# Kernel optimization log

Hardware: AMD Instinct MI355X
Metric: run time of the kernel (lower is better)

The kernel has to match this reference:

```python
import jax, jax.numpy as jnp
import numpy as np

B, N, L, D = 4, 32, 64, 512      # batch, num_nodes, his_len, input_dim
H, O = 1024, 512                  # expert hidden, output_dim
E, S, TOP_K = 16, 3, 2            # independent experts, shared experts, top-k


def setup_inputs() -> dict:
    key = jax.random.key(0)
    ks = jax.random.split(key, 12)
    sc = 0.02
    return {
        "feature_vectors": jax.random.normal(ks[0], (B, N, L, D), jnp.float32),
        "object_types": jax.random.uniform(ks[1], (B, N, L, S, 1), jnp.float32),
        "gating_w": jax.random.normal(ks[2], (D, E), jnp.float32) * sc,
        "gating_b": jnp.zeros((E,), jnp.float32),
        "sh_w1": jax.random.normal(ks[3], (S, D, H), jnp.float32) * sc,
        "sh_b1": jnp.zeros((S, H), jnp.float32),
        "sh_w2": jax.random.normal(ks[4], (S, H, O), jnp.float32) * sc,
        "sh_b2": jnp.zeros((S, O), jnp.float32),
        "ind_w1": jax.random.normal(ks[5], (E, D, H), jnp.float32) * sc,
        "ind_b1": jnp.zeros((E, H), jnp.float32),
        "ind_w2": jax.random.normal(ks[6], (E, H, O), jnp.float32) * sc,
        "ind_b2": jnp.zeros((E, O), jnp.float32),
    }


def reference(feature_vectors, object_types, gating_w, gating_b,
              sh_w1, sh_b1, sh_w2, sh_b2,
              ind_w1, ind_b1, ind_w2, ind_b2):
    b, n, l, d = feature_vectors.shape
    x = feature_vectors.reshape(-1, d)                       # [T, D]
    T = x.shape[0]

    # gating: softmax -> top-k -> renormalize selected weights
    gating = jax.nn.softmax(x @ gating_w + gating_b, axis=-1)  # [T, E]
    vals, idx = jax.lax.top_k(gating, TOP_K)                   # [T, K]
    w = vals / vals.sum(axis=-1, keepdims=True)                # [T, K]

    # shared experts: per-type FFN, weighted by object_types
    obj = object_types.reshape(-1, S, 1)                       # [T, S, 1]
    sh_h = jax.nn.relu(jnp.einsum('td,sdh->tsh', x, sh_w1) + sh_b1)
    sh_o = jnp.einsum('tsh,sho->tso', sh_h, sh_w2) + sh_b2     # [T, S, O]
    shared_out = (sh_o * obj).sum(axis=1)                      # [T, O]

    # independent experts: dense all-expert compute, combine via top-k weights
    # (equivalent to the bincount/mask dispatch loop: unselected experts get 0)
    ind_h = jax.nn.relu(jnp.einsum('td,edh->teh', x, ind_w1) + ind_b1)
    ind_o = jnp.einsum('teh,eho->teo', ind_h, ind_w2) + ind_b2  # [T, E, O]
    comb = jnp.zeros((T, gating_w.shape[1]), x.dtype)
    comb = comb.at[jnp.arange(T)[:, None], idx].add(w)          # [T, E] sparse weights
    ind_out = jnp.einsum('te,teo->to', comb, ind_o)             # [T, O]

    out = 0.5 * shared_out + 0.5 * ind_out
    return out.reshape(b, n, l, -1)
```

## Files before the change

kernel.cpp:

```cpp
#include <hip/hip_runtime.h>
#include <hip/hip_bf16.h>
#include <stdint.h>

#define T_TOK 8192
#define DIM   512
#define HID   1024
#define ODIM  512
#define NEXP  16
#define NSH   3

#define BM 128
#define BN 128
#define BK 64
#define MAXTILES 144
#define CAPSLOTS (MAXTILES * BM)

typedef __attribute__((ext_vector_type(8))) short s16x8;
typedef __attribute__((ext_vector_type(4))) float f32x4;

__device__ __forceinline__ uint16_t f2bf(float f) {
  union { float f; uint32_t u; } x; x.f = f;
  uint32_t r = x.u + 0x7FFFu + ((x.u >> 16) & 1u);
  return (uint16_t)(r >> 16);
}
__device__ __forceinline__ float bf2f(uint16_t u) {
  union { uint32_t u; float f; } x; x.u = ((uint32_t)u) << 16;
  return x.f;
}

__device__ __forceinline__ void async_copy16(const uint16_t* g, uint16_t* l) {
  __builtin_amdgcn_global_load_lds(
      (const __attribute__((address_space(1))) void*)g,
      (__attribute__((address_space(3))) void*)l, 16, 0, 0);
}

__global__ __launch_bounds__(256) void k_cvt_all(
    const float* __restrict__ shw1, const float* __restrict__ shw2,
    const float* __restrict__ iw1, const float* __restrict__ iw2,
    uint16_t* __restrict__ shw1T, uint16_t* __restrict__ shw2T,
    uint16_t* __restrict__ iw1T, uint16_t* __restrict__ iw2T) {
  __shared__ float tl[64][68];
  int id = blockIdx.x;
  const float* src; uint16_t* dst; int K, N, ldk; size_t dz;
  if (id < 384)       { src = shw1; dst = shw1T; K = 512;  N = 1024; dz = (size_t)HID * DIM;  ldk = 512; }
  else if (id < 768)  { src = shw2; dst = shw2T; K = 1024; N = 512;  dz = HID;                ldk = 3072; id -= 384; }
  else if (id < 2816) { src = iw1;  dst = iw1T;  K = 512;  N = 1024; dz = (size_t)HID * DIM;  ldk = 512;  id -= 768; }
  else                { src = iw2;  dst = iw2T;  K = 1024; N = 512;  dz = (size_t)ODIM * HID; ldk = 1024; id -= 2816; }
  int z = id >> 7, tile = id & 127;
  int ntn = N >> 6;
  int n0 = (tile & (ntn - 1)) * 64, k0 = (tile / ntn) * 64;
  src += (size_t)z * K * N;
  dst += (size_t)z * dz;
  int tid = threadIdx.x;
  int lr = tid >> 4, lc = (tid & 15) * 4;
#pragma unroll
  for (int p = 0; p < 4; ++p) {
    int row = lr + p * 16;
    float4 v = *(const float4*)&src[(size_t)(k0 + row) * N + n0 + lc];
    tl[row][lc + 0] = v.x; tl[row][lc + 1] = v.y;
    tl[row][lc + 2] = v.z; tl[row][lc + 3] = v.w;
  }
  __syncthreads();
  int nr = tid >> 3, kc = (tid & 7) * 8;
#pragma unroll
  for (int p = 0; p < 2; ++p) {
    int n = nr + p * 32;
    s16x8 o;
#pragma unroll
    for (int j = 0; j < 8; ++j) o[j] = (short)f2bf(tl[kc + j][n]);
    *(s16x8*)&dst[(size_t)(n0 + n) * ldk + k0 + kc] = o;
  }
}

#define GTPB 16
__global__ __launch_bounds__(256) void k_gating(const float* __restrict__ x,
                                                const float* __restrict__ gw,
                                                const float* __restrict__ gb,
                                                uint16_t* __restrict__ xb,
                                                int* __restrict__ tok_top,
                                                float* __restrict__ wgt_top,
                                                int* __restrict__ cnt) {
  __shared__ float xs[GTPB][516];
  __shared__ float gws[NEXP][516];
  __shared__ int hist[NEXP];
  int tid = threadIdx.x;
  int tb = blockIdx.x * GTPB;
  if (tid < NEXP) hist[tid] = 0;
#pragma unroll
  for (int it = 0; it < 8; ++it) {
    int idx = (it * 256 + tid) * 4;
    float4 v = *(const float4*)&gw[idx];
    int d = idx >> 4, e0 = idx & 15;
    gws[e0 + 0][d] = v.x; gws[e0 + 1][d] = v.y;
    gws[e0 + 2][d] = v.z; gws[e0 + 3][d] = v.w;
  }
#pragma unroll
  for (int it = 0; it < 8; ++it) {
    int idx = it * 1024 + tid * 4;
    float4 v = *(const float4*)&x[(size_t)tb * DIM + idx];
    *(float4*)&xs[idx >> 9][idx & 511] = v;
  }
  __syncthreads();
#pragma unroll
  for (int it = 0; it < 4; ++it) {
    int idx = it * 2048 + tid * 8;
    int row = idx >> 9, col = idx & 511;
    float4 v0 = *(const float4*)&xs[row][col];
    float4 v1 = *(const float4*)&xs[row][col + 4];
    ushort4 o0, o1;
    o0.x = f2bf(v0.x); o0.y = f2bf(v0.y); o0.z = f2bf(v0.z); o0.w = f2bf(v0.w);
    o1.x = f2bf(v1.x); o1.y = f2bf(v1.y); o1.z = f2bf(v1.z); o1.w = f2bf(v1.w);
    *(ushort4*)&xb[(size_t)(tb + row) * DIM + col] = o0;
    *(ushort4*)&xb[(size_t)(tb + row) * DIM + col + 4] = o1;
  }
  int tok = tid >> 4, e = tid & 15;
  float acc = 0.f;
#pragma unroll 8
  for (int k = 0; k < DIM / 4; ++k) {
    float4 xv = *(const float4*)&xs[tok][k * 4];
    float4 gv = *(const float4*)&gws[e][k * 4];
    acc += xv.x * gv.x + xv.y * gv.y + xv.z * gv.z + xv.w * gv.w;
  }
  acc += gb[e];
  int lbase = (tid & 63) & 48;
  float best1 = -3.4e38f; int i1 = 0;
#pragma unroll
  for (int ee = 0; ee < NEXP; ++ee) {
    float v = __shfl(acc, lbase + ee, 64);
    if (v > best1) { best1 = v; i1 = ee; }
  }
  float best2 = -3.4e38f; int i2 = 0;
#pragma unroll
  for (int ee = 0; ee < NEXP; ++ee) {
    float v = __shfl(acc, lbase + ee, 64);
    if (ee != i1 && v > best2) { best2 = v; i2 = ee; }
  }
  if (e == 0) {
    int t = tb + tok;
    float w0 = 1.f / (1.f + expf(best2 - best1));
    tok_top[t * 2] = i1; tok_top[t * 2 + 1] = i2;
    wgt_top[t * 2] = w0; wgt_top[t * 2 + 1] = 1.f - w0;
    atomicAdd(&hist[i1], 1);
    atomicAdd(&hist[i2], 1);
  }
  __syncthreads();
  if (tid < NEXP && hist[tid]) atomicAdd(&cnt[tid], hist[tid]);
}

__global__ __launch_bounds__(256) void k_sched(const int* __restrict__ cnt,
                                               int* __restrict__ eoff,
                                               int* __restrict__ tdesc,
                                               int* __restrict__ ntl,
                                               int* __restrict__ rowtok,
                                               int* __restrict__ fill) {
  if (threadIdx.x == 0) {
    int o = 0, nt = 0;
    for (int e = 0; e < NEXP; ++e) {
      eoff[e] = o;
      int c = cnt[e];
      int t = (c + BM - 1) >> 7;
      for (int i = 0; i < t; ++i) { tdesc[nt * 2] = e; tdesc[nt * 2 + 1] = o + i * BM; ++nt; }
      o += t << 7;
      fill[e] = 0;
    }
    eoff[NEXP] = o;
    *ntl = nt;
  }
  for (int i = threadIdx.x; i < CAPSLOTS; i += 256) rowtok[i] = -1;
}

__global__ __launch_bounds__(256) void k_fill(const int* __restrict__ tok_top,
                                              const int* __restrict__ eoff,
                                              int* __restrict__ fill,
                                              int* __restrict__ rowtok,
                                              int* __restrict__ tok2slot) {
  int t = blockIdx.x * 256 + threadIdx.x;
  if (t >= T_TOK) return;
#pragma unroll
  for (int k = 0; k < 2; ++k) {
    int e = tok_top[t * 2 + k];
    int p = atomicAdd(&fill[e], 1);
    int slot = eoff[e] + p;
    rowtok[slot] = t;
    tok2slot[t * 2 + k] = slot;
  }
}

__device__ __forceinline__ void gemm_core(
    const uint16_t* a0, const uint16_t* a1, const uint16_t* a2, const uint16_t* a3,
    const uint16_t* b0, const uint16_t* b1, const uint16_t* b2, const uint16_t* b3,
    int nsteps, uint16_t* As, uint16_t* Bs, int wlds,
    int tl, int th, int wr, int wc, f32x4 (&acc)[4][4]) {
  const int sw = (tl & 7) << 3;
  for (int ks = 0; ks < nsteps; ++ks) {
    async_copy16(a0, As + wlds);           async_copy16(a1, As + wlds + 8 * BK);
    async_copy16(a2, As + wlds + 16 * BK); async_copy16(a3, As + wlds + 24 * BK);
    async_copy16(b0, Bs + wlds);           async_copy16(b1, Bs + wlds + 8 * BK);
    async_copy16(b2, Bs + wlds + 16 * BK); async_copy16(b3, Bs + wlds + 24 * BK);
    __syncthreads();
#pragma unroll
    for (int kk = 0; kk < 2; ++kk) {
      s16x8 af[4], bf[4];
#pragma unroll
      for (int i = 0; i < 4; ++i) {
        int eo = (kk * 32 + th * 8) ^ sw;
        af[i] = *(const s16x8*)&As[(wr * 64 + i * 16 + tl) * BK + eo];
        bf[i] = *(const s16x8*)&Bs[(wc * 64 + i * 16 + tl) * BK + eo];
      }
#pragma unroll
      for (int i = 0; i < 4; ++i)
#pragma unroll
        for (int j = 0; j < 4; ++j)
          acc[i][j] = __builtin_amdgcn_mfma_f32_16x16x32_bf16(af[i], bf[j], acc[i][j], 0, 0, 0);
    }
    __syncthreads();
    a0 += BK; a1 += BK; a2 += BK; a3 += BK;
    b0 += BK; b1 += BK; b2 += BK; b3 += BK;
  }
}

__global__ __launch_bounds__(256) void k_mega1(
    const uint16_t* __restrict__ xb, const uint16_t* __restrict__ shw1T,
    const float* __restrict__ shb1, const float* __restrict__ obj,
    uint16_t* __restrict__ hbuf,
    const int* __restrict__ tdesc, const int* __restrict__ ntl,
    const int* __restrict__ rowtok, const uint16_t* __restrict__ iw1T,
    const float* __restrict__ ib1, uint16_t* __restrict__ hind) {
  __shared__ uint16_t As[BM * BK], Bs[BN * BK];
  int id = blockIdx.x;
  int tid = threadIdx.x, lane = tid & 63, wid = tid >> 6;
  int wr = wid >> 1, wc = wid & 1, tl = lane & 15, th = lane >> 4;
  int lr = wid * 32 + (lane >> 3), koff = ((lane & 7) ^ (lane >> 3)) * 8;
  int wlds = wid * 32 * BK;
  f32x4 acc[4][4] = {};
  if (id < 1536) {
    int xcd = id & 7, g = id >> 3;
    int m0 = (xcd * 8 + g / 24) * BM;
    int n0 = (g % 24) * BN;
    const uint16_t* a0 = xb + (size_t)(m0 + lr) * DIM + koff;
    const uint16_t* b0 = shw1T + (size_t)(n0 + lr) * DIM + koff;
    gemm_core(a0, a0 + 8 * DIM, a0 + 16 * DIM, a0 + 24 * DIM,
              b0, b0 + 8 * DIM, b0 + 16 * DIM, b0 + 24 * DIM,
              DIM / BK, As, Bs, wlds, tl, th, wr, wc, acc);
#pragma unroll
    for (int i = 0; i < 4; ++i)
#pragma unroll
      for (int j = 0; j < 4; ++j) {
        int col = n0 + wc * 64 + j * 16 + tl;
        int s = col >> 10;
        float bv = shb1[col];
#pragma unroll
        for (int q = 0; q < 4; ++q) {
          int row = m0 + wr * 64 + i * 16 + th * 4 + q;
          float v = acc[i][j][q] + bv;
          float ow = 0.5f * obj[row * NSH + s];
          hbuf[(size_t)row * (NSH * HID) + col] = f2bf(ow * (v > 0.f ? v : 0.f));
        }
      }
  } else {
    int id2 = id - 1536;
    int xcd = id2 & 7, g = id2 >> 3;
    int t = xcd * 18 + (g >> 3);
    int n0 = (g & 7) * BN;
    if (t >= *ntl) return;
    int e = tdesc[t * 2], slot0 = tdesc[t * 2 + 1];
    const uint16_t* Bt = iw1T + (size_t)e * HID * DIM;
    const uint16_t* ap[4];
#pragma unroll
    for (int i = 0; i < 4; ++i) {
      int tk = rowtok[slot0 + lr + i * 8];
      if (tk < 0) tk = 0;
      ap[i] = xb + (size_t)tk * DIM + koff;
    }
    const uint16_t* b0 = Bt + (size_t)(n0 + lr) * DIM + koff;
    gemm_core(ap[0], ap[1], ap[2], ap[3],
              b0, b0 + 8 * DIM, b0 + 16 * DIM, b0 + 24 * DIM,
              DIM / BK, As, Bs, wlds, tl, th, wr, wc, acc);
#pragma unroll
    for (int i = 0; i < 4; ++i)
#pragma unroll
      for (int j = 0; j < 4; ++j) {
        int col = n0 + wc * 64 + j * 16 + tl;
        float bv = ib1[e * HID + col];
#pragma unroll
        for (int q = 0; q < 4; ++q) {
          int rowl = wr * 64 + i * 16 + th * 4 + q;
          float v = acc[i][j][q] + bv;
          hind[(size_t)(slot0 + rowl) * HID + col] = f2bf(v > 0.f ? v : 0.f);
        }
      }
  }
}

__global__ __launch_bounds__(256) void k_mega2(
    const uint16_t* __restrict__ hbuf, const uint16_t* __restrict__ shw2T,
    const float* __restrict__ shb2, const float* __restrict__ obj,
    float* __restrict__ outp,
    const int* __restrict__ tdesc, const int* __restrict__ ntl,
    const uint16_t* __restrict__ hind, const uint16_t* __restrict__ iw2T,
    const float* __restrict__ ib2,
    uint16_t* __restrict__ pind) {
  __shared__ uint16_t As[BM * BK], Bs[BN * BK];
  int id = blockIdx.x;
  int tid = threadIdx.x, lane = tid & 63, wid = tid >> 6;
  int wr = wid >> 1, wc = wid & 1, tl = lane & 15, th = lane >> 4;
  int lr = wid * 32 + (lane >> 3), koff = ((lane & 7) ^ (lane >> 3)) * 8;
  int wlds = wid * 32 * BK;
  f32x4 acc[4][4] = {};
  if (id < 256) {
    const int K = NSH * HID;
    int xcd = id & 7, g = id >> 3;
    int m0 = (xcd * 8 + (g >> 2)) * BM;
    int n0 = (g & 3) * BN;
    const uint16_t* a0 = hbuf + (size_t)(m0 + lr) * K + koff;
    const uint16_t* b0 = shw2T + (size_t)(n0 + lr) * K + koff;
    gemm_core(a0, a0 + 8 * K, a0 + 16 * K, a0 + 24 * K,
              b0, b0 + 8 * K, b0 + 16 * K, b0 + 24 * K,
              K / BK, As, Bs, wlds, tl, th, wr, wc, acc);
#pragma unroll
    for (int i = 0; i < 4; ++i) {
      int rows[4]; float ob[4][NSH];
#pragma unroll
      for (int q = 0; q < 4; ++q) {
        rows[q] = m0 + wr * 64 + i * 16 + th * 4 + q;
#pragma unroll
        for (int s = 0; s < NSH; ++s) ob[q][s] = 0.5f * obj[rows[q] * NSH + s];
      }
#pragma unroll
      for (int j = 0; j < 4; ++j) {
        int col = n0 + wc * 64 + j * 16 + tl;
#pragma unroll
        for (int q = 0; q < 4; ++q) {
          float v = acc[i][j][q];
#pragma unroll
          for (int s = 0; s < NSH; ++s) v += ob[q][s] * shb2[s * ODIM + col];
          outp[(size_t)rows[q] * ODIM + col] = v;
        }
      }
    }
  } else {
    int id2 = id - 256;
    int xcd = id2 & 7, g = id2 >> 3;
    int t = xcd * 18 + (g >> 2);
    int n0 = (g & 3) * BN;
    if (t >= *ntl) return;
    int e = tdesc[t * 2], slot0 = tdesc[t * 2 + 1];
    const uint16_t* a0 = hind + (size_t)(slot0 + lr) * HID + koff;
    const uint16_t* b0 = iw2T + (size_t)e * ODIM * HID + (size_t)(n0 + lr) * HID + koff;
    gemm_core(a0, a0 + 8 * HID, a0 + 16 * HID, a0 + 24 * HID,
              b0, b0 + 8 * HID, b0 + 16 * HID, b0 + 24 * HID,
              HID / BK, As, Bs, wlds, tl, th, wr, wc, acc);
#pragma unroll
    for (int i = 0; i < 4; ++i)
#pragma unroll
      for (int j = 0; j < 4; ++j) {
        int col = n0 + wc * 64 + j * 16 + tl;
        float bv = ib2[e * ODIM + col];
#pragma unroll
        for (int q = 0; q < 4; ++q) {
          int slot = slot0 + wr * 64 + i * 16 + th * 4 + q;
          pind[(size_t)slot * ODIM + col] = f2bf(acc[i][j][q] + bv);
        }
      }
  }
}

__global__ __launch_bounds__(256) void k_combine(float* __restrict__ outp,
                                                 const uint16_t* __restrict__ pind,
                                                 const int* __restrict__ tok2slot,
                                                 const float* __restrict__ wgt_top) {
  int t = blockIdx.x * 4 + (threadIdx.x >> 6);
  int c = (threadIdx.x & 63) * 8;
  int s0 = tok2slot[t * 2], s1 = tok2slot[t * 2 + 1];
  float w0 = 0.5f * wgt_top[t * 2], w1 = 0.5f * wgt_top[t * 2 + 1];
  s16x8 p0 = *(const s16x8*)&pind[(size_t)s0 * ODIM + c];
  s16x8 p1 = *(const s16x8*)&pind[(size_t)s1 * ODIM + c];
  float* op = &outp[(size_t)t * ODIM + c];
  float4 o0 = *(float4*)op, o1 = *(float4*)(op + 4);
  float r[8];
#pragma unroll
  for (int j = 0; j < 8; ++j)
    r[j] = w0 * bf2f((uint16_t)p0[j]) + w1 * bf2f((uint16_t)p1[j]);
  o0.x += r[0]; o0.y += r[1]; o0.z += r[2]; o0.w += r[3];
  o1.x += r[4]; o1.y += r[5]; o1.z += r[6]; o1.w += r[7];
  *(float4*)op = o0; *(float4*)(op + 4) = o1;
}

extern "C" void kernel_launch(void* const* d_in, const int* in_sizes, int n_in,
                              void* d_out, int out_size, void* d_ws, size_t ws_size,
                              hipStream_t stream) {
  (void)in_sizes; (void)n_in; (void)out_size; (void)ws_size;
  const float* fv   = (const float*)d_in[0];
  const float* obj  = (const float*)d_in[1];
  const float* gw   = (const float*)d_in[2];
  const float* gb   = (const float*)d_in[3];
  const float* shw1 = (const float*)d_in[4];
  const float* shb1 = (const float*)d_in[5];
  const float* shw2 = (const float*)d_in[6];
  const float* shb2 = (const float*)d_in[7];
  const float* iw1  = (const float*)d_in[8];
  const float* ib1  = (const float*)d_in[9];
  const float* iw2  = (const float*)d_in[10];
  const float* ib2  = (const float*)d_in[11];
  float* outp = (float*)d_out;

  char* w = (char*)d_ws;
  size_t off = 0;
  auto alloc = [&](size_t bytes) {
    char* p = w + off;
    off = (off + bytes + 255) & ~(size_t)255;
    return p;
  };
  uint16_t* xb    = (uint16_t*)alloc((size_t)T_TOK * DIM * 2);
  uint16_t* hbuf  = (uint16_t*)alloc((size_t)T_TOK * NSH * HID * 2);
  uint16_t* hind  = (uint16_t*)alloc((size_t)CAPSLOTS * HID * 2);
  uint16_t* pind  = (uint16_t*)alloc((size_t)CAPSLOTS * ODIM * 2);
  uint16_t* shw1T = (uint16_t*)alloc((size_t)NSH * HID * DIM * 2);
  uint16_t* shw2T = (uint16_t*)alloc((size_t)ODIM * NSH * HID * 2);
  uint16_t* iw1T  = (uint16_t*)alloc((size_t)NEXP * HID * DIM * 2);
  uint16_t* iw2T  = (uint16_t*)alloc((size_t)NEXP * ODIM * HID * 2);
  int*   tok_top  = (int*)alloc(T_TOK * 2 * 4);
  float* wgt_top  = (float*)alloc(T_TOK * 2 * 4);
  int*   tok2slot = (int*)alloc(T_TOK * 2 * 4);
  int*   rowtok   = (int*)alloc(CAPSLOTS * 4);
  int*   cnt      = (int*)alloc(64);
  int*   fill     = (int*)alloc(64);
  int*   eoff     = (int*)alloc((NEXP + 1) * 4);
  int*   tdesc    = (int*)alloc(MAXTILES * 2 * 4);
  int*   ntl      = (int*)alloc(4);

  hipMemsetAsync(cnt, 0, 64, stream);
  k_cvt_all<<<4864, 256, 0, stream>>>(shw1, shw2, iw1, iw2, shw1T, shw2T, iw1T, iw2T);
  k_gating<<<T_TOK / GTPB, 256, 0, stream>>>(fv, gw, gb, xb, tok_top, wgt_top, cnt);
  k_sched<<<1, 256, 0, stream>>>(cnt, eoff, tdesc, ntl, rowtok, fill);
  k_fill<<<T_TOK / 256, 256, 0, stream>>>(tok_top, eoff, fill, rowtok, tok2slot);

  k_mega1<<<1536 + 8 * MAXTILES, 256, 0, stream>>>(
      xb, shw1T, shb1, obj, hbuf, tdesc, ntl, rowtok, iw1T, ib1, hind);
  k_mega2<<<256 + 4 * MAXTILES, 256, 0, stream>>>(
      hbuf, shw2T, shb2, obj, outp, tdesc, ntl, hind, iw2T, ib2, pind);
  k_combine<<<T_TOK / 4, 256, 0, stream>>>(outp, pind, tok2slot, wgt_top);
}
```

Measured before the change: 228.2 us.

## Split shared-expert down-proj GEMM along K per expert to raise block count

The shared-expert second GEMM (K=3072) is split into three K=1024 GEMMs, one per shared expert, tripling the number of blocks from 256 to 768. Expert 0 writes fp32 to the output and experts 1 and 2 write bf16 partials, which the combine kernel then sums. This targets the low parallelism and long serial K loop of the old 256-block shared GEMM. In exchange it adds extra global traffic for the two bf16 partial buffers and an additional rounding step.

```diff
diff --git a/kernel.cpp b/kernel.cpp
--- a/kernel.cpp
+++ b/kernel.cpp
@@ -299,50 +299,51 @@
     const int* __restrict__ tdesc, const int* __restrict__ ntl,
     const uint16_t* __restrict__ hind, const uint16_t* __restrict__ iw2T,
     const float* __restrict__ ib2,
+    uint16_t* __restrict__ p1, uint16_t* __restrict__ p2,
     uint16_t* __restrict__ pind) {
   __shared__ uint16_t As[BM * BK], Bs[BN * BK];
   int id = blockIdx.x;
+  int xcd = id & 7, g = id >> 3;
   int tid = threadIdx.x, lane = tid & 63, wid = tid >> 6;
   int wr = wid >> 1, wc = wid & 1, tl = lane & 15, th = lane >> 4;
   int lr = wid * 32 + (lane >> 3), koff = ((lane & 7) ^ (lane >> 3)) * 8;
   int wlds = wid * 32 * BK;
   f32x4 acc[4][4] = {};
-  if (id < 256) {
+  if (g < 96) {
     const int K = NSH * HID;
-    int xcd = id & 7, g = id >> 3;
-    int m0 = (xcd * 8 + (g >> 2)) * BM;
-    int n0 = (g & 3) * BN;
-    const uint16_t* a0 = hbuf + (size_t)(m0 + lr) * K + koff;
-    const uint16_t* b0 = shw2T + (size_t)(n0 + lr) * K + koff;
+    int m0 = (xcd * 8 + g / 12) * BM;
+    int r = g % 12, s = r >> 2, n0 = (r & 3) * BN;
+    const uint16_t* a0 = hbuf + (size_t)(m0 + lr) * K + s * HID + koff;
+    const uint16_t* b0 = shw2T + (size_t)(n0 + lr) * K + s * HID + koff;
     gemm_core(a0, a0 + 8 * K, a0 + 16 * K, a0 + 24 * K,
               b0, b0 + 8 * K, b0 + 16 * K, b0 + 24 * K,
-              K / BK, As, Bs, wlds, tl, th, wr, wc, acc);
+              HID / BK, As, Bs, wlds, tl, th, wr, wc, acc);
 #pragma unroll
     for (int i = 0; i < 4; ++i) {
-      int rows[4]; float ob[4][NSH];
+      int rows[4]; float ow[4];
 #pragma unroll
       for (int q = 0; q < 4; ++q) {
         rows[q] = m0 + wr * 64 + i * 16 + th * 4 + q;
-#pragma unroll
-        for (int s = 0; s < NSH; ++s) ob[q][s] = 0.5f * obj[rows[q] * NSH + s];
+        ow[q] = 0.5f * obj[rows[q] * NSH + s];
       }
 #pragma unroll
       for (int j = 0; j < 4; ++j) {
         int col = n0 + wc * 64 + j * 16 + tl;
+        float bv = shb2[s * ODIM + col];
 #pragma unroll
         for (int q = 0; q < 4; ++q) {
-          float v = acc[i][j][q];
-#pragma unroll
-          for (int s = 0; s < NSH; ++s) v += ob[q][s] * shb2[s * ODIM + col];
-          outp[(size_t)rows[q] * ODIM + col] = v;
+          float v = acc[i][j][q] + ow[q] * bv;
+          size_t idx = (size_t)rows[q] * ODIM + col;
+          if (s == 0)      outp[idx] = v;
+          else if (s == 1) p1[idx] = f2bf(v);
+          else             p2[idx] = f2bf(v);
         }
       }
     }
   } else {
-    int id2 = id - 256;
-    int xcd = id2 & 7, g = id2 >> 3;
-    int t = xcd * 18 + (g >> 2);
-    int n0 = (g & 3) * BN;
+    int g2 = g - 96;
+    int t = xcd * 18 + (g2 >> 2);
+    int n0 = (g2 & 3) * BN;
     if (t >= *ntl) return;
     int e = tdesc[t * 2], slot0 = tdesc[t * 2 + 1];
     const uint16_t* a0 = hind + (size_t)(slot0 + lr) * HID + koff;
@@ -366,6 +367,8 @@
 }
 
 __global__ __launch_bounds__(256) void k_combine(float* __restrict__ outp,
+                                                 const uint16_t* __restrict__ p1,
+                                                 const uint16_t* __restrict__ p2,
                                                  const uint16_t* __restrict__ pind,
                                                  const int* __restrict__ tok2slot,
                                                  const float* __restrict__ wgt_top) {
@@ -373,14 +376,18 @@
   int c = (threadIdx.x & 63) * 8;
   int s0 = tok2slot[t * 2], s1 = tok2slot[t * 2 + 1];
   float w0 = 0.5f * wgt_top[t * 2], w1 = 0.5f * wgt_top[t * 2 + 1];
+  size_t tc = (size_t)t * ODIM + c;
+  s16x8 q1 = *(const s16x8*)&p1[tc];
+  s16x8 q2 = *(const s16x8*)&p2[tc];
   s16x8 p0 = *(const s16x8*)&pind[(size_t)s0 * ODIM + c];
-  s16x8 p1 = *(const s16x8*)&pind[(size_t)s1 * ODIM + c];
-  float* op = &outp[(size_t)t * ODIM + c];
+  s16x8 pq = *(const s16x8*)&pind[(size_t)s1 * ODIM + c];
+  float* op = &outp[tc];
   float4 o0 = *(float4*)op, o1 = *(float4*)(op + 4);
   float r[8];
 #pragma unroll
   for (int j = 0; j < 8; ++j)
-    r[j] = w0 * bf2f((uint16_t)p0[j]) + w1 * bf2f((uint16_t)p1[j]);
+    r[j] = bf2f((uint16_t)q1[j]) + bf2f((uint16_t)q2[j]) +
+           w0 * bf2f((uint16_t)p0[j]) + w1 * bf2f((uint16_t)pq[j]);
   o0.x += r[0]; o0.y += r[1]; o0.z += r[2]; o0.w += r[3];
   o1.x += r[4]; o1.y += r[5]; o1.z += r[6]; o1.w += r[7];
   *(float4*)op = o0; *(float4*)(op + 4) = o1;
@@ -415,6 +422,8 @@
   uint16_t* hbuf  = (uint16_t*)alloc((size_t)T_TOK * NSH * HID * 2);
   uint16_t* hind  = (uint16_t*)alloc((size_t)CAPSLOTS * HID * 2);
   uint16_t* pind  = (uint16_t*)alloc((size_t)CAPSLOTS * ODIM * 2);
+  uint16_t* p1    = (uint16_t*)alloc((size_t)T_TOK * ODIM * 2);
+  uint16_t* p2    = (uint16_t*)alloc((size_t)T_TOK * ODIM * 2);
   uint16_t* shw1T = (uint16_t*)alloc((size_t)NSH * HID * DIM * 2);
   uint16_t* shw2T = (uint16_t*)alloc((size_t)ODIM * NSH * HID * 2);
   uint16_t* iw1T  = (uint16_t*)alloc((size_t)NEXP * HID * DIM * 2);
@@ -437,7 +446,7 @@
 
   k_mega1<<<1536 + 8 * MAXTILES, 256, 0, stream>>>(
       xb, shw1T, shb1, obj, hbuf, tdesc, ntl, rowtok, iw1T, ib1, hind);
-  k_mega2<<<256 + 4 * MAXTILES, 256, 0, stream>>>(
-      hbuf, shw2T, shb2, obj, outp, tdesc, ntl, hind, iw2T, ib2, pind);
-  k_combine<<<T_TOK / 4, 256, 0, stream>>>(outp, pind, tok2slot, wgt_top);
-}
+  k_mega2<<<1344, 256, 0, stream>>>(
+      hbuf, shw2T, shb2, obj, outp, tdesc, ntl, hind, iw2T, ib2, p1, p2, pind);
+  k_combine<<<T_TOK / 4, 256, 0, stream>>>(outp, p1, p2, pind, tok2slot, wgt_top);
+}
```

Measured after the change: 239.0 us. +4.7%, slower.

## Merge weight conversion with gating and fuse scheduling with slot fill

Applied to the files above, without the earlier changes.

Weight transpose/convert and gating now run as two block ranges inside one launch that shares a union of shared-memory layouts. The histogram, tile schedule and slot fill move into a single-block kernel that counts from tok_top with shared-memory atomics. This drops a memset and two kernel launches, cutting launch gaps between the small pre-processing stages. In exchange, the fill step is serialized onto one workgroup over 16K entries, and the union raises shared-memory use for the convert blocks.

```diff
diff --git a/kernel.cpp b/kernel.cpp
--- a/kernel.cpp
+++ b/kernel.cpp
@@ -34,155 +34,146 @@
       (__attribute__((address_space(3))) void*)l, 16, 0, 0);
 }
 
-__global__ __launch_bounds__(256) void k_cvt_all(
+#define GTPB 16
+
+union PreSmem {
+  float tl[64][69];
+  struct { float xs[GTPB][516]; float gws[NEXP][516]; } g;
+};
+
+__global__ __launch_bounds__(256) void k_pre(
     const float* __restrict__ shw1, const float* __restrict__ shw2,
     const float* __restrict__ iw1, const float* __restrict__ iw2,
     uint16_t* __restrict__ shw1T, uint16_t* __restrict__ shw2T,
-    uint16_t* __restrict__ iw1T, uint16_t* __restrict__ iw2T) {
-  __shared__ float tl[64][68];
-  int id = blockIdx.x;
-  const float* src; uint16_t* dst; int K, N, ldk; size_t dz;
-  if (id < 384)       { src = shw1; dst = shw1T; K = 512;  N = 1024; dz = (size_t)HID * DIM;  ldk = 512; }
-  else if (id < 768)  { src = shw2; dst = shw2T; K = 1024; N = 512;  dz = HID;                ldk = 3072; id -= 384; }
-  else if (id < 2816) { src = iw1;  dst = iw1T;  K = 512;  N = 1024; dz = (size_t)HID * DIM;  ldk = 512;  id -= 768; }
-  else                { src = iw2;  dst = iw2T;  K = 1024; N = 512;  dz = (size_t)ODIM * HID; ldk = 1024; id -= 2816; }
-  int z = id >> 7, tile = id & 127;
-  int ntn = N >> 6;
-  int n0 = (tile & (ntn - 1)) * 64, k0 = (tile / ntn) * 64;
-  src += (size_t)z * K * N;
-  dst += (size_t)z * dz;
+    uint16_t* __restrict__ iw1T, uint16_t* __restrict__ iw2T,
+    const float* __restrict__ x, const float* __restrict__ gw,
+    const float* __restrict__ gb, uint16_t* __restrict__ xb,
+    int* __restrict__ tok_top, float* __restrict__ wgt_top) {
+  __shared__ PreSmem sm;
   int tid = threadIdx.x;
-  int lr = tid >> 4, lc = (tid & 15) * 4;
-#pragma unroll
-  for (int p = 0; p < 4; ++p) {
-    int row = lr + p * 16;
-    float4 v = *(const float4*)&src[(size_t)(k0 + row) * N + n0 + lc];
-    tl[row][lc + 0] = v.x; tl[row][lc + 1] = v.y;
-    tl[row][lc + 2] = v.z; tl[row][lc + 3] = v.w;
-  }
+  if (blockIdx.x < 4864) {
+    int id = blockIdx.x;
+    const float* src; uint16_t* dst; int K, N, ldk; size_t dz;
+    if (id < 384)       { src = shw1; dst = shw1T; K = 512;  N = 1024; dz = (size_t)HID * DIM;  ldk = 512; }
+    else if (id < 768)  { src = shw2; dst = shw2T; K = 1024; N = 512;  dz = HID;                ldk = 3072; id -= 384; }
+    else if (id < 2816) { src = iw1;  dst = iw1T;  K = 512;  N = 1024; dz = (size_t)HID * DIM;  ldk = 512;  id -= 768; }
+    else                { src = iw2;  dst = iw2T;  K = 1024; N = 512;  dz = (size_t)ODIM * HID; ldk = 1024; id -= 2816; }
+    int z = id >> 7, tile = id & 127;
+    int ntn = N >> 6;
+    int n0 = (tile & (ntn - 1)) * 64, k0 = (tile / ntn) * 64;
+    src += (size_t)z * K * N;
+    dst += (size_t)z * dz;
+    int lr = tid >> 4, lc = (tid & 15) * 4;
+#pragma unroll
+    for (int p = 0; p < 4; ++p) {
+      int row = lr + p * 16;
+      float4 v = *(const float4*)&src[(size_t)(k0 + row) * N + n0 + lc];
+      sm.tl[row][lc + 0] = v.x; sm.tl[row][lc + 1] = v.y;
+      sm.tl[row][lc + 2] = v.z; sm.tl[row][lc + 3] = v.w;
+    }
+    __syncthreads();
+    int nr = tid >> 3, kc = (tid & 7) * 8;
+#pragma unroll
+    for (int p = 0; p < 2; ++p) {
+      int n = nr + p * 32;
+      s16x8 o;
+#pragma unroll
+      for (int j = 0; j < 8; ++j) o[j] = (short)f2bf(sm.tl[kc + j][n]);
+      *(s16x8*)&dst[(size_t)(n0 + n) * ldk + k0 + kc] = o;
+    }
+  } else {
+    int tb = (blockIdx.x - 4864) * GTPB;
+#pragma unroll
+    for (int it = 0; it < 8; ++it) {
+      int idx = (it * 256 + tid) * 4;
+      float4 v = *(const float4*)&gw[idx];
+      int d = idx >> 4, e0 = idx & 15;
+      sm.g.gws[e0 + 0][d] = v.x; sm.g.gws[e0 + 1][d] = v.y;
+      sm.g.gws[e0 + 2][d] = v.z; sm.g.gws[e0 + 3][d] = v.w;
+    }
+#pragma unroll
+    for (int it = 0; it < 8; ++it) {
+      int idx = it * 1024 + tid * 4;
+      float4 v = *(const float4*)&x[(size_t)tb * DIM + idx];
+      *(float4*)&sm.g.xs[idx >> 9][idx & 511] = v;
+    }
+    __syncthreads();
+#pragma unroll
+    for (int it = 0; it < 4; ++it) {
+      int idx = it * 2048 + tid * 8;
+      int row = idx >> 9, col = idx & 511;
+      float4 v0 = *(const float4*)&sm.g.xs[row][col];
+      float4 v1 = *(const float4*)&sm.g.xs[row][col + 4];
+      ushort4 o0, o1;
+      o0.x = f2bf(v0.x); o0.y = f2bf(v0.y); o0.z = f2bf(v0.z); o0.w = f2bf(v0.w);
+      o1.x = f2bf(v1.x); o1.y = f2bf(v1.y); o1.z = f2bf(v1.z); o1.w = f2bf(v1.w);
+      *(ushort4*)&xb[(size_t)(tb + row) * DIM + col] = o0;
+      *(ushort4*)&xb[(size_t)(tb + row) * DIM + col + 4] = o1;
+    }
+    int tok = tid >> 4, e = tid & 15;
+    float acc = 0.f;
+#pragma unroll 8
+    for (int k = 0; k < DIM / 4; ++k) {
+      float4 xv = *(const float4*)&sm.g.xs[tok][k * 4];
+      float4 gv = *(const float4*)&sm.g.gws[e][k * 4];
+      acc += xv.x * gv.x + xv.y * gv.y + xv.z * gv.z + xv.w * gv.w;
+    }
+    acc += gb[e];
+    int lbase = (tid & 63) & 48;
+    float best1 = -3.4e38f; int i1 = 0;
+#pragma unroll
+    for (int ee = 0; ee < NEXP; ++ee) {
+      float v = __shfl(acc, lbase + ee, 64);
+      if (v > best1) { best1 = v; i1 = ee; }
+    }
+    float best2 = -3.4e38f; int i2 = 0;
+#pragma unroll
+    for (int ee = 0; ee < NEXP; ++ee) {
+      float v = __shfl(acc, lbase + ee, 64);
+      if (ee != i1 && v > best2) { best2 = v; i2 = ee; }
+    }
+    if (e == 0) {
+      int t = tb + tok;
+      float w0 = 1.f / (1.f + expf(best2 - best1));
+      tok_top[t * 2] = i1; tok_top[t * 2 + 1] = i2;
+      wgt_top[t * 2] = w0; wgt_top[t * 2 + 1] = 1.f - w0;
+    }
+  }
+}
+
+__global__ __launch_bounds__(256) void k_schedfill(
+    const int* __restrict__ tok_top,
+    int* __restrict__ tdesc, int* __restrict__ ntl,
+    int* __restrict__ rowtok, int* __restrict__ tok2slot) {
+  __shared__ int hist[NEXP], seoff[NEXP], sfill[NEXP];
+  int tid = threadIdx.x;
+  if (tid < NEXP) hist[tid] = 0;
+  for (int i = tid; i < CAPSLOTS; i += 256) rowtok[i] = -1;
   __syncthreads();
-  int nr = tid >> 3, kc = (tid & 7) * 8;
-#pragma unroll
-  for (int p = 0; p < 2; ++p) {
-    int n = nr + p * 32;
-    s16x8 o;
-#pragma unroll
-    for (int j = 0; j < 8; ++j) o[j] = (short)f2bf(tl[kc + j][n]);
-    *(s16x8*)&dst[(size_t)(n0 + n) * ldk + k0 + kc] = o;
-  }
-}
-
-#define GTPB 16
-__global__ __launch_bounds__(256) void k_gating(const float* __restrict__ x,
-                                                const float* __restrict__ gw,
-                                                const float* __restrict__ gb,
-                                                uint16_t* __restrict__ xb,
-                                                int* __restrict__ tok_top,
-                                                float* __restrict__ wgt_top,
-                                                int* __restrict__ cnt) {
-  __shared__ float xs[GTPB][516];
-  __shared__ float gws[NEXP][516];
-  __shared__ int hist[NEXP];
-  int tid = threadIdx.x;
-  int tb = blockIdx.x * GTPB;
-  if (tid < NEXP) hist[tid] = 0;
-#pragma unroll
-  for (int it = 0; it < 8; ++it) {
-    int idx = (it * 256 + tid) * 4;
-    float4 v = *(const float4*)&gw[idx];
-    int d = idx >> 4, e0 = idx & 15;
-    gws[e0 + 0][d] = v.x; gws[e0 + 1][d] = v.y;
-    gws[e0 + 2][d] = v.z; gws[e0 + 3][d] = v.w;
-  }
-#pragma unroll
-  for (int it = 0; it < 8; ++it) {
-    int idx = it * 1024 + tid * 4;
-    float4 v = *(const float4*)&x[(size_t)tb * DIM + idx];
-    *(float4*)&xs[idx >> 9][idx & 511] = v;
-  }
+  for (int i = tid; i < T_TOK * 2; i += 256) atomicAdd(&hist[tok_top[i]], 1);
   __syncthreads();
-#pragma unroll
-  for (int it = 0; it < 4; ++it) {
-    int idx = it * 2048 + tid * 8;
-    int row = idx >> 9, col = idx & 511;
-    float4 v0 = *(const float4*)&xs[row][col];
-    float4 v1 = *(const float4*)&xs[row][col + 4];
-    ushort4 o0, o1;
-    o0.x = f2bf(v0.x); o0.y = f2bf(v0.y); o0.z = f2bf(v0.z); o0.w = f2bf(v0.w);
-    o1.x = f2bf(v1.x); o1.y = f2bf(v1.y); o1.z = f2bf(v1.z); o1.w = f2bf(v1.w);
-    *(ushort4*)&xb[(size_t)(tb + row) * DIM + col] = o0;
-    *(ushort4*)&xb[(size_t)(tb + row) * DIM + col + 4] = o1;
-  }
-  int tok = tid >> 4, e = tid & 15;
-  float acc = 0.f;
-#pragma unroll 8
-  for (int k = 0; k < DIM / 4; ++k) {
-    float4 xv = *(const float4*)&xs[tok][k * 4];
-    float4 gv = *(const float4*)&gws[e][k * 4];
-    acc += xv.x * gv.x + xv.y * gv.y + xv.z * gv.z + xv.w * gv.w;
-  }
-  acc += gb[e];
-  int lbase = (tid & 63) & 48;
-  float best1 = -3.4e38f; int i1 = 0;
-#pragma unroll
-  for (int ee = 0; ee < NEXP; ++ee) {
-    float v = __shfl(acc, lbase + ee, 64);
-    if (v > best1) { best1 = v; i1 = ee; }
-  }
-  float best2 = -3.4e38f; int i2 = 0;
-#pragma unroll
-  for (int ee = 0; ee < NEXP; ++ee) {
-    float v = __shfl(acc, lbase + ee, 64);
-    if (ee != i1 && v > best2) { best2 = v; i2 = ee; }
-  }
-  if (e == 0) {
-    int t = tb + tok;
-    float w0 = 1.f / (1.f + expf(best2 - best1));
-    tok_top[t * 2] = i1; tok_top[t * 2 + 1] = i2;
-    wgt_top[t * 2] = w0; wgt_top[t * 2 + 1] = 1.f - w0;
-    atomicAdd(&hist[i1], 1);
-    atomicAdd(&hist[i2], 1);
-  }
-  __syncthreads();
-  if (tid < NEXP && hist[tid]) atomicAdd(&cnt[tid], hist[tid]);
-}
-
-__global__ __launch_bounds__(256) void k_sched(const int* __restrict__ cnt,
-                                               int* __restrict__ eoff,
-                                               int* __restrict__ tdesc,
-                                               int* __restrict__ ntl,
-                                               int* __restrict__ rowtok,
-                                               int* __restrict__ fill) {
-  if (threadIdx.x == 0) {
+  if (tid == 0) {
     int o = 0, nt = 0;
     for (int e = 0; e < NEXP; ++e) {
-      eoff[e] = o;
-      int c = cnt[e];
+      seoff[e] = o;
+      int c = hist[e];
       int t = (c + BM - 1) >> 7;
       for (int i = 0; i < t; ++i) { tdesc[nt * 2] = e; tdesc[nt * 2 + 1] = o + i * BM; ++nt; }
       o += t << 7;
-      fill[e] = 0;
-    }
-    eoff[NEXP] = o;
+    }
     *ntl = nt;
   }
-  for (int i = threadIdx.x; i < CAPSLOTS; i += 256) rowtok[i] = -1;
-}
-
-__global__ __launch_bounds__(256) void k_fill(const int* __restrict__ tok_top,
-                                              const int* __restrict__ eoff,
-                                              int* __restrict__ fill,
-                                              int* __restrict__ rowtok,
-                                              int* __restrict__ tok2slot) {
-  int t = blockIdx.x * 256 + threadIdx.x;
-  if (t >= T_TOK) return;
-#pragma unroll
-  for (int k = 0; k < 2; ++k) {
-    int e = tok_top[t * 2 + k];
-    int p = atomicAdd(&fill[e], 1);
-    int slot = eoff[e] + p;
-    rowtok[slot] = t;
-    tok2slot[t * 2 + k] = slot;
+  if (tid < NEXP) sfill[tid] = 0;
+  __syncthreads();
+  for (int t = tid; t < T_TOK; t += 256) {
+#pragma unroll
+    for (int k = 0; k < 2; ++k) {
+      int e = tok_top[t * 2 + k];
+      int p = atomicAdd(&sfill[e], 1);
+      int slot = seoff[e] + p;
+      rowtok[slot] = t;
+      tok2slot[t * 2 + k] = slot;
+    }
   }
 }
 
@@ -423,17 +414,12 @@
   float* wgt_top  = (float*)alloc(T_TOK * 2 * 4);
   int*   tok2slot = (int*)alloc(T_TOK * 2 * 4);
   int*   rowtok   = (int*)alloc(CAPSLOTS * 4);
-  int*   cnt      = (int*)alloc(64);
-  int*   fill     = (int*)alloc(64);
-  int*   eoff     = (int*)alloc((NEXP + 1) * 4);
   int*   tdesc    = (int*)alloc(MAXTILES * 2 * 4);
   int*   ntl      = (int*)alloc(4);
 
-  hipMemsetAsync(cnt, 0, 64, stream);
-  k_cvt_all<<<4864, 256, 0, stream>>>(shw1, shw2, iw1, iw2, shw1T, shw2T, iw1T, iw2T);
-  k_gating<<<T_TOK / GTPB, 256, 0, stream>>>(fv, gw, gb, xb, tok_top, wgt_top, cnt);
-  k_sched<<<1, 256, 0, stream>>>(cnt, eoff, tdesc, ntl, rowtok, fill);
-  k_fill<<<T_TOK / 256, 256, 0, stream>>>(tok_top, eoff, fill, rowtok, tok2slot);
+  k_pre<<<5376, 256, 0, stream>>>(shw1, shw2, iw1, iw2, shw1T, shw2T, iw1T, iw2T,
+                                  fv, gw, gb, xb, tok_top, wgt_top);
+  k_schedfill<<<1, 256, 0, stream>>>(tok_top, tdesc, ntl, rowtok, tok2slot);
 
   k_mega1<<<1536 + 8 * MAXTILES, 256, 0, stream>>>(
       xb, shw1T, shb1, obj, hbuf, tdesc, ntl, rowtok, iw1T, ib1, hind);
```

Result: faster. 202.6 us (-11.2%).
